# Optimization experiments

Hardware: AMD Instinct MI355X
Metric: run time of the kernel (lower is better)

The kernel has to match this reference:

```python
import jax, jax.numpy as jnp
import numpy as np

R = 2  # decimation factor


def _cheby1_sos(N=8, rp=0.05, Wn=1.0 / R):
    """Chebyshev type-I lowpass, second-order sections (matches scipy.signal.cheby1 math)."""
    eps = np.sqrt(10.0 ** (rp / 10.0) - 1.0)
    mu = np.arcsinh(1.0 / eps) / N
    k = np.arange(1, N + 1)
    theta = np.pi * (2 * k - 1) / (2 * N)
    # analog prototype poles (no zeros)
    p = -np.sinh(mu) * np.sin(theta) + 1j * np.cosh(mu) * np.cos(theta)
    gain = np.real(np.prod(-p))
    if N % 2 == 0:
        gain /= np.sqrt(1.0 + eps * eps)
    # prewarp + lp2lp
    fs = 2.0
    warped = 2.0 * fs * np.tan(np.pi * Wn / fs)
    p = p * warped
    gain = gain * warped ** N
    # bilinear transform (zeros -> z=-1, order N)
    fs2 = 2.0 * fs
    pz = (fs2 + p) / (fs2 - p)
    gain = gain / np.real(np.prod(fs2 - p))
    # pair complex-conjugate poles into biquads (N even, all complex)
    pp = pz[np.imag(pz) > 0]
    a1 = -2.0 * np.real(pp)
    a2 = np.abs(pp) ** 2
    g = gain ** (1.0 / len(pp))  # distribute gain evenly across sections
    b0 = np.full(len(pp), g)
    sos = np.stack([b0, 2.0 * b0, b0, np.ones(len(pp)), a1, a2], axis=1)
    return sos  # [nsec, 6] float64


_SOS = _cheby1_sos()


def _sosfilt(x):
    """Cascaded biquads, direct form II transposed, zero initial state. x: [B, T]."""
    B = x.shape[0]
    nsec = _SOS.shape[0]
    b0 = jnp.asarray(_SOS[:, 0], x.dtype)
    b1 = jnp.asarray(_SOS[:, 1], x.dtype)
    b2 = jnp.asarray(_SOS[:, 2], x.dtype)
    a1 = jnp.asarray(_SOS[:, 4], x.dtype)
    a2 = jnp.asarray(_SOS[:, 5], x.dtype)

    def step(carry, xt):  # carry: (z1, z2) each [B, nsec]; xt: [B]
        z1, z2 = carry
        y = xt
        nz1, nz2 = [], []
        for s in range(nsec):  # fixed small unroll over sections
            out = b0[s] * y + z1[:, s]
            nz1.append(b1[s] * y + z2[:, s] - a1[s] * out)
            nz2.append(b2[s] * y - a2[s] * out)
            y = out
        return (jnp.stack(nz1, axis=1), jnp.stack(nz2, axis=1)), y

    z0 = jnp.zeros((B, nsec), x.dtype)
    _, ys = jax.lax.scan(step, (z0, z0), x.T)  # scan over time
    return ys.T  # [B, T]


def setup_inputs() -> dict:
    key = jax.random.key(0)
    x = jax.random.normal(key, (32, 131072), dtype=jnp.float32)
    return {"x": x}


def reference(x) -> jnp.ndarray:
    y = _sosfilt(x)
    return y[..., ::R]
```

## Files before the change

kernel.cpp:

```cpp
#include <hip/hip_runtime.h>
#include <cmath>
#include <complex>


#define T_LEN   131072
#define B_ROWS  32
#define OUT_LEN (T_LEN / 2)
#define L_CHUNK 64
#define H_WARM  128
#define TPB     256
#define BLOCKS_PER_ROW (T_LEN / (L_CHUNK * TPB))
#define WIN_FLOATS (TPB * L_CHUNK + H_WARM)
#define WIN_UNITS  (WIN_FLOATS / 4)
#define LDS_UNITS  (WIN_UNITS + 8)
#define NBLOCKS (B_ROWS * BLOCKS_PER_ROW)

typedef float v2f __attribute__((ext_vector_type(2)));

#if defined(__has_builtin)
# if __has_builtin(__builtin_elementwise_fma)
#  define FMA2(a, b, c) __builtin_elementwise_fma((a), (b), (c))
# endif
#endif
#ifndef FMA2
static __device__ __forceinline__ v2f fma2_(v2f a, v2f b, v2f c) {
    v2f r; r.x = fmaf(a.x, b.x, c.x); r.y = fmaf(a.y, b.y, c.y); return r;
}
# define FMA2 fma2_
#endif

struct Coef { float g; float a1[4]; float a2[4]; };

__global__ __launch_bounds__(256) void cheby_decimate_kernel(
    const float* __restrict__ x, float* __restrict__ out, Coef c)
{
    __shared__ float4 lds[LDS_UNITS];
    const int t   = threadIdx.x;
    const int row = blockIdx.x / BLOCKS_PER_ROW;
    const int bc  = blockIdx.x % BLOCKS_PER_ROW;
    const float* __restrict__ xr = x + (size_t)row * T_LEN;
    const int wstart = bc * (TPB * L_CHUNK) - H_WARM;

    #pragma unroll
    for (int k = 0; k < (WIN_UNITS + TPB - 1) / TPB; ++k) {
        int w = t + TPB * k;
        if (w < WIN_UNITS) {
            int g = wstart + 4 * w;
            float4 v = make_float4(0.f, 0.f, 0.f, 0.f);
            if (g >= 0) v = *reinterpret_cast<const float4*>(xr + g);
            lds[w ^ ((w >> 4) & 7)] = v;
        }
    }
    if (t < 8)
        lds[WIN_UNITS + t] = make_float4(0.f, 0.f, 0.f, 0.f);
    __syncthreads();

    const v2f gg   = { c.g, c.g };
    const v2f two  = { 2.f, 2.f };
    const v2f naA1 = { -c.a1[0], -c.a1[2] }, naA2 = { -c.a2[0], -c.a2[2] };
    const v2f naB1 = { -c.a1[1], -c.a1[3] }, naB2 = { -c.a2[1], -c.a2[3] };

    v2f zA1 = {0.f,0.f}, zA2 = {0.f,0.f}, zB1 = {0.f,0.f}, zB2 = {0.f,0.f};
    v2f o13 = {0.f,0.f}, o24 = {0.f,0.f};

#define LREAD(u) lds[(u) ^ (((u) >> 4) & 7)]
#define PSTEP(xi, STORE) do {                                                  \
        v2f i13; i13.x = (xi); i13.y = o24.x;                                  \
        v2f i24 = o13;                                                         \
        v2f wA = gg * i13; v2f oA = wA + zA1; v2f tA = FMA2(two, wA, zA2);     \
        zA1 = FMA2(naA1, oA, tA); zA2 = FMA2(naA2, oA, wA);                    \
        v2f wB = gg * i24; v2f oB = wB + zB1; v2f tB = FMA2(two, wB, zB2);     \
        zB1 = FMA2(naB1, oB, tB); zB2 = FMA2(naB2, oB, wB);                    \
        o13 = oA; o24 = oB; STORE;                                             \
    } while (0)

    const int ub = 16 * t;
    float4 cur = LREAD(ub);
    float outv[32];

    #pragma unroll 4
    for (int m = 0; m < 32; ++m) {
        float4 nxt = LREAD(ub + m + 1);
        PSTEP(cur.x, (void)0); PSTEP(cur.y, (void)0);
        PSTEP(cur.z, (void)0); PSTEP(cur.w, (void)0);
        cur = nxt;
    }
    #pragma unroll
    for (int m = 32; m <= 48; ++m) {
        float4 nxt = (m < 48) ? LREAD(ub + m + 1)
                              : make_float4(0.f, 0.f, 0.f, 0.f);
        PSTEP(cur.x, (void)0);
        PSTEP(cur.y, if (m >= 33) outv[2*m - 65] = o24.y);
        PSTEP(cur.z, (void)0);
        PSTEP(cur.w, if (m <= 47) outv[2*m - 64] = o24.y);
        cur = nxt;
    }
#undef PSTEP
#undef LREAD

    float* __restrict__ op = out + (size_t)row * OUT_LEN
                                 + (size_t)bc * (TPB * L_CHUNK / 2) + 32 * t;
    #pragma unroll
    for (int q = 0; q < 8; ++q) {
        *reinterpret_cast<float4*>(op + 4 * q) =
            make_float4(outv[4*q], outv[4*q+1], outv[4*q+2], outv[4*q+3]);
    }
}

extern "C" void kernel_launch(void* const* d_in, const int* in_sizes, int n_in,
                              void* d_out, int out_size, void* d_ws, size_t ws_size,
                              hipStream_t stream)
{
    const float* x = (const float*)d_in[0];
    float* out = (float*)d_out;

    const int N = 8;
    const double rp = 0.05;
    const double eps = std::sqrt(std::pow(10.0, rp / 10.0) - 1.0);
    const double mu  = std::asinh(1.0 / eps) / N;

    std::complex<double> p[8];
    std::complex<double> prodnp(1.0, 0.0);
    for (int i = 0; i < N; ++i) {
        double theta = M_PI * (2.0 * (i + 1) - 1.0) / (2.0 * N);
        p[i] = std::complex<double>(-std::sinh(mu) * std::sin(theta),
                                     std::cosh(mu) * std::cos(theta));
        prodnp *= -p[i];
    }
    double gain = prodnp.real() / std::sqrt(1.0 + eps * eps);

    const double fs = 2.0;
    const double warped = 2.0 * fs * std::tan(M_PI * 0.5 / fs);
    std::complex<double> prodden(1.0, 0.0);
    std::complex<double> pz[8];
    for (int i = 0; i < N; ++i) {
        p[i] *= warped;
        pz[i] = (2.0 * fs + p[i]) / (2.0 * fs - p[i]);
        prodden *= (2.0 * fs - p[i]);
    }
    gain *= std::pow(warped, (double)N);
    gain /= prodden.real();

    Coef c;
    int ns = 0;
    double A1[4], A2[4];
    for (int i = 0; i < N; ++i) {
        if (pz[i].imag() > 0.0) {
            A1[ns] = -2.0 * pz[i].real();
            A2[ns] = std::norm(pz[i]);
            ++ns;
        }
    }
    const double gsec = std::pow(gain, 1.0 / ns);
    c.g = (float)gsec;
    for (int s = 0; s < 4; ++s) { c.a1[s] = (float)A1[s]; c.a2[s] = (float)A2[s]; }

    dim3 block(TPB), grid(NBLOCKS);
    hipLaunchKernelGGL(cheby_decimate_kernel, grid, block, 0, stream, x, out, c);
}
```

Before: 72.06 us.

## Stream inputs from global memory via per-thread register ring instead of LDS staging

Drops the shared-memory window load, swizzle and block barrier. Each thread now reads its own warm-up plus chunk span straight from global memory, keeping an 8-deep float4 register prefetch ring. This removes LDS traffic and the sync, but each thread now makes strided, uncoalesced 16-byte loads that are 256 B apart across lanes. It also uses more registers and relies on the cache to absorb the overlapping warm-up reads.

```diff
diff --git a/kernel.cpp b/kernel.cpp
--- a/kernel.cpp
+++ b/kernel.cpp
@@ -9,11 +9,10 @@
 #define L_CHUNK 64
 #define H_WARM  128
 #define TPB     256
-#define BLOCKS_PER_ROW (T_LEN / (L_CHUNK * TPB))
-#define WIN_FLOATS (TPB * L_CHUNK + H_WARM)
-#define WIN_UNITS  (WIN_FLOATS / 4)
-#define LDS_UNITS  (WIN_UNITS + 8)
-#define NBLOCKS (B_ROWS * BLOCKS_PER_ROW)
+#define CPR     (T_LEN / L_CHUNK)
+#define NBLOCKS (B_ROWS * CPR / TPB)
+#define WUNITS  ((H_WARM + L_CHUNK) / 4)
+#define DEPTH   8
 
 typedef float v2f __attribute__((ext_vector_type(2)));
 
@@ -34,26 +33,12 @@
 __global__ __launch_bounds__(256) void cheby_decimate_kernel(
     const float* __restrict__ x, float* __restrict__ out, Coef c)
 {
-    __shared__ float4 lds[LDS_UNITS];
-    const int t   = threadIdx.x;
-    const int row = blockIdx.x / BLOCKS_PER_ROW;
-    const int bc  = blockIdx.x % BLOCKS_PER_ROW;
-    const float* __restrict__ xr = x + (size_t)row * T_LEN;
-    const int wstart = bc * (TPB * L_CHUNK) - H_WARM;
-
-    #pragma unroll
-    for (int k = 0; k < (WIN_UNITS + TPB - 1) / TPB; ++k) {
-        int w = t + TPB * k;
-        if (w < WIN_UNITS) {
-            int g = wstart + 4 * w;
-            float4 v = make_float4(0.f, 0.f, 0.f, 0.f);
-            if (g >= 0) v = *reinterpret_cast<const float4*>(xr + g);
-            lds[w ^ ((w >> 4) & 7)] = v;
-        }
-    }
-    if (t < 8)
-        lds[WIN_UNITS + t] = make_float4(0.f, 0.f, 0.f, 0.f);
-    __syncthreads();
+    const int tid   = blockIdx.x * TPB + threadIdx.x;
+    const int row   = tid >> 11;
+    const int chunk = tid & (CPR - 1);
+    const float4* __restrict__ xu =
+        reinterpret_cast<const float4*>(x + (size_t)row * T_LEN);
+    const int u0 = 16 * chunk - H_WARM / 4;
 
     const v2f gg   = { c.g, c.g };
     const v2f two  = { 2.f, 2.f };
@@ -63,7 +48,15 @@
     v2f zA1 = {0.f,0.f}, zA2 = {0.f,0.f}, zB1 = {0.f,0.f}, zB2 = {0.f,0.f};
     v2f o13 = {0.f,0.f}, o24 = {0.f,0.f};
 
-#define LREAD(u) lds[(u) ^ (((u) >> 4) & 7)]
+    const float4 zf4 = make_float4(0.f, 0.f, 0.f, 0.f);
+
+    float4 ring[DEPTH];
+    #pragma unroll
+    for (int k = 0; k < DEPTH; ++k) {
+        int g = u0 + k;
+        ring[k] = (g >= 0) ? xu[g] : zf4;
+    }
+
 #define PSTEP(xi, STORE) do {                                                  \
         v2f i13; i13.x = (xi); i13.y = o24.x;                                  \
         v2f i24 = o13;                                                         \
@@ -74,32 +67,28 @@
         o13 = oA; o24 = oB; STORE;                                             \
     } while (0)
 
-    const int ub = 16 * t;
-    float4 cur = LREAD(ub);
     float outv[32];
 
-    #pragma unroll 4
+    #pragma unroll 8
     for (int m = 0; m < 32; ++m) {
-        float4 nxt = LREAD(ub + m + 1);
+        float4 cur = ring[m & (DEPTH - 1)];
+        int g = u0 + m + DEPTH;
+        ring[m & (DEPTH - 1)] = (g >= 0) ? xu[g] : zf4;
         PSTEP(cur.x, (void)0); PSTEP(cur.y, (void)0);
         PSTEP(cur.z, (void)0); PSTEP(cur.w, (void)0);
-        cur = nxt;
     }
     #pragma unroll
     for (int m = 32; m <= 48; ++m) {
-        float4 nxt = (m < 48) ? LREAD(ub + m + 1)
-                              : make_float4(0.f, 0.f, 0.f, 0.f);
+        float4 cur = ring[m & (DEPTH - 1)];
+        ring[m & (DEPTH - 1)] = (m + DEPTH < WUNITS) ? xu[u0 + m + DEPTH] : zf4;
         PSTEP(cur.x, (void)0);
         PSTEP(cur.y, if (m >= 33) outv[2*m - 65] = o24.y);
         PSTEP(cur.z, (void)0);
         PSTEP(cur.w, if (m <= 47) outv[2*m - 64] = o24.y);
-        cur = nxt;
     }
 #undef PSTEP
-#undef LREAD
 
-    float* __restrict__ op = out + (size_t)row * OUT_LEN
-                                 + (size_t)bc * (TPB * L_CHUNK / 2) + 32 * t;
+    float* __restrict__ op = out + (size_t)row * OUT_LEN + 32 * (size_t)chunk;
     #pragma unroll
     for (int q = 0; q < 8; ++q) {
         *reinterpret_cast<float4*>(op + 4 * q) =
```

Measured after the change: 91.15 us. 26.5% more time.
